# Performance work log

Hardware: AMD Instinct MI355X
Metric: run time of the kernel (lower is better)

Reference implementation:

```python
import jax, jax.numpy as jnp
import numpy as np

B, Q, K, H, D = 2, 2048, 2048, 16, 64


def setup_inputs() -> dict:
    key = jax.random.key(0)
    k1, k2, k3, k4 = jax.random.split(key, 4)
    qs = jax.random.normal(k1, (B, Q, H, D), dtype=jnp.float32)
    ks = jax.random.normal(k2, (B, K, H, D), dtype=jnp.float32)
    vs = jax.random.normal(k3, (B, K, H, D), dtype=jnp.float32)
    # valid lengths in [1, K] so no row is fully masked
    valid_lens = jax.random.randint(k4, (B,), 1, K + 1, dtype=jnp.int32)
    return {"qs": qs, "ks": ks, "vs": vs, "valid_lens": valid_lens}


def reference(qs, ks, vs, valid_lens):
    # Flash-attention-2 scan computes exact softmax attention with key masking;
    # the dense, numerically-stable equivalent:
    d = qs.shape[-1]
    scale = 1.0 / jnp.sqrt(jnp.asarray(d, dtype=qs.dtype))
    # scores: [B, H, Q, K]
    scores = jnp.einsum("bqhd,bkhd->bhqk", qs * scale, ks)
    kpos = jnp.arange(ks.shape[1])
    ks_mask = kpos[None, :] < valid_lens[:, None]            # [B, K]
    scores = jnp.where(ks_mask[:, None, None, :], scores, -jnp.inf)
    attn = jax.nn.softmax(scores, axis=-1)                   # stable online-softmax equivalent
    out = jnp.einsum("bhqk,bkhd->bqhd", attn, vs)            # [B, Q, H, D]
    return out
```

## Files before the change

### kernel.cpp

```cpp
#include <hip/hip_runtime.h>

#define B_ 2
#define Q_ 2048
#define K_ 2048
#define H_ 16
#define D_ 64
#define HD_ (H_ * D_)

#define QSCALE 0.18033688011112042f
#define DEFER_THR 10.0f

typedef __bf16 bf16_t;
typedef __attribute__((ext_vector_type(8))) __bf16 bf16x8;
typedef __attribute__((ext_vector_type(4))) __bf16 bf16x4;
typedef __attribute__((ext_vector_type(4))) float f32x4;

#define SBAR() do {                                         \
    __builtin_amdgcn_sched_barrier(0);                      \
    asm volatile("s_waitcnt lgkmcnt(0)" ::: "memory");      \
    __builtin_amdgcn_s_barrier();                           \
    __builtin_amdgcn_sched_barrier(0);                      \
} while (0)

__device__ __forceinline__ int swz(int row, int colByte) {
    return (row * 128 + colByte) ^ ((row & 7) << 4);
}

__global__ __launch_bounds__(512, 4) void attn_fwd_kernel(
    const float* __restrict__ qs, const float* __restrict__ ks,
    const float* __restrict__ vs, const int* __restrict__ valid_lens,
    float* __restrict__ out)
{
    const int qt   = blockIdx.x;
    const int h    = blockIdx.y;
    const int b    = blockIdx.z;
    const int tid  = threadIdx.x;
    const int wave = tid >> 6;
    const int lane = tid & 63;
    const int l16  = lane & 15;
    const int lhi  = lane >> 4;

    const int valid  = valid_lens[b];
    const int ntiles = (valid + 63) >> 6;

    __shared__ bf16_t k_lds[2][64 * 64];
    __shared__ bf16_t v_lds[2][64 * 64];
    __shared__ bf16_t p_buf[8][16 * 64];
    char* const pbase = (char*)&p_buf[wave][0];

    const int    qrow = qt * 128 + wave * 16 + l16;
    const float* qp   = qs + (((size_t)b * Q_ + qrow) * H_ + h) * D_;
    bf16x8 a_q[2];
    #pragma unroll
    for (int dh = 0; dh < 2; ++dh) {
        const f32x4* q4 = (const f32x4*)(qp + dh * 32 + lhi * 8);
        f32x4 lo = q4[0], hi = q4[1];
        #pragma unroll
        for (int j = 0; j < 4; ++j) {
            a_q[dh][j]     = (bf16_t)(lo[j] * QSCALE);
            a_q[dh][4 + j] = (bf16_t)(hi[j] * QSCALE);
        }
    }

    f32x4 o_acc[4];
    #pragma unroll
    for (int t = 0; t < 4; ++t) o_acc[t] = (f32x4){0.f, 0.f, 0.f, 0.f};
    float m_r = -1e30f, l_part = 0.f;

    const float* kb = ks + ((size_t)b * K_ * H_ + h) * D_;
    const float* vg = vs + ((size_t)b * K_ * H_ + h) * D_;

    const bool kRole = (tid < 256);
    const int  st    = kRole ? tid : (tid - 256);
    const int  krow  = st >> 2;
    const int  kcolf = (st & 3) * 16;
    const int  vr    = (st & 15) * 4;
    const int  vc    = (st >> 4) * 4;

    f32x4 reg[4];

    auto issue_loads = [&](int kt) {
        if (kRole) {
            const float* ksrc = kb + (size_t)(kt * 64 + krow) * HD_ + kcolf;
            #pragma unroll
            for (int i = 0; i < 4; ++i) reg[i] = ((const f32x4*)ksrc)[i];
        } else {
            #pragma unroll
            for (int i = 0; i < 4; ++i)
                reg[i] = *(const f32x4*)(vg + (size_t)(kt * 64 + vr + i) * HD_ + vc);
        }
    };

    auto write_tile = [&](int bi) {
        if (kRole) {
            char* kdst = (char*)&k_lds[bi][0];
            bf16x8 lo, hi;
            #pragma unroll
            for (int j = 0; j < 4; ++j) {
                lo[j] = (bf16_t)reg[0][j]; lo[4 + j] = (bf16_t)reg[1][j];
                hi[j] = (bf16_t)reg[2][j]; hi[4 + j] = (bf16_t)reg[3][j];
            }
            *(bf16x8*)(kdst + swz(krow, kcolf * 2))      = lo;
            *(bf16x8*)(kdst + swz(krow, kcolf * 2 + 16)) = hi;
        } else {
            char* vdst = (char*)&v_lds[bi][0];
            #pragma unroll
            for (int j = 0; j < 4; ++j) {
                bf16x4 w;
                w[0] = (bf16_t)reg[0][j]; w[1] = (bf16_t)reg[1][j];
                w[2] = (bf16_t)reg[2][j]; w[3] = (bf16_t)reg[3][j];
                *(bf16x4*)(vdst + swz(vc + j, vr * 2)) = w;
            }
        }
    };

    issue_loads(0);
    write_tile(0);
    int cur = 0;

    for (int kt = 0; kt < ntiles; ++kt) {
        const bool more = (kt + 1 < ntiles);
        if (more) issue_loads(kt + 1);
        SBAR();

        char* const kbase = (char*)&k_lds[cur][0];
        char* const vbase = (char*)&v_lds[cur][0];

        f32x4 s[4];
        #pragma unroll
        for (int n = 0; n < 4; ++n) s[n] = (f32x4){0.f, 0.f, 0.f, 0.f};
        __builtin_amdgcn_s_setprio(1);
        #pragma unroll
        for (int n = 0; n < 4; ++n) {
            #pragma unroll
            for (int dh = 0; dh < 2; ++dh) {
                bf16x8 ak = *(const bf16x8*)(kbase + swz(n * 16 + l16, dh * 64 + lhi * 16));
                s[n] = __builtin_amdgcn_mfma_f32_16x16x32_bf16(ak, a_q[dh], s[n], 0, 0, 0);
            }
        }
        __builtin_amdgcn_s_setprio(0);

        if (kt * 64 + 64 > valid) {
            #pragma unroll
            for (int n = 0; n < 4; ++n) {
                const int kbase_i = kt * 64 + n * 16 + lhi * 4;
                #pragma unroll
                for (int r = 0; r < 4; ++r)
                    if (kbase_i + r >= valid) s[n][r] = -1e30f;
            }
        }

        float lm = s[0][0];
        #pragma unroll
        for (int n = 0; n < 4; ++n)
            #pragma unroll
            for (int r = 0; r < 4; ++r) lm = fmaxf(lm, s[n][r]);
        if (__any(lm > m_r + DEFER_THR)) {
            float rm = fmaxf(lm, __shfl_xor(lm, 16, 64));
            rm = fmaxf(rm, __shfl_xor(rm, 32, 64));
            const float mnew  = fmaxf(m_r, rm);
            const float alpha = __builtin_amdgcn_exp2f(m_r - mnew);
            m_r = mnew;
            l_part *= alpha;
            #pragma unroll
            for (int t = 0; t < 4; ++t) o_acc[t] *= alpha;
        }
        float psum = 0.f;
        #pragma unroll
        for (int n = 0; n < 4; ++n) {
            bf16x4 w;
            #pragma unroll
            for (int r = 0; r < 4; ++r) {
                const float e = __builtin_amdgcn_exp2f(s[n][r] - m_r);
                psum += e;
                w[r] = (bf16_t)e;
            }
            *(bf16x4*)(pbase + swz(l16, n * 32 + lhi * 8)) = w;
        }
        l_part += psum;

        bf16x8 pb[2];
        #pragma unroll
        for (int kk = 0; kk < 2; ++kk)
            pb[kk] = *(const bf16x8*)(pbase + swz(l16, kk * 64 + lhi * 16));

        __builtin_amdgcn_s_setprio(1);
        #pragma unroll
        for (int t = 0; t < 4; ++t) {
            #pragma unroll
            for (int kk = 0; kk < 2; ++kk) {
                bf16x8 vb = *(const bf16x8*)(vbase + swz(t * 16 + l16, kk * 64 + lhi * 16));
                o_acc[t] = __builtin_amdgcn_mfma_f32_16x16x32_bf16(vb, pb[kk], o_acc[t], 0, 0, 0);
            }
        }
        __builtin_amdgcn_s_setprio(0);

        if (more) write_tile(cur ^ 1);
        cur ^= 1;
    }

    float l = l_part;
    l += __shfl_xor(l, 16, 64);
    l += __shfl_xor(l, 32, 64);
    const float inv = 1.f / l;
    float* op = out + (((size_t)b * Q_ + qrow) * H_ + h) * D_;
    #pragma unroll
    for (int t = 0; t < 4; ++t) {
        f32x4 res = o_acc[t];
        #pragma unroll
        for (int r = 0; r < 4; ++r) res[r] *= inv;
        *(f32x4*)(op + t * 16 + lhi * 4) = res;
    }
}

extern "C" void kernel_launch(void* const* d_in, const int* in_sizes, int n_in,
                              void* d_out, int out_size, void* d_ws, size_t ws_size,
                              hipStream_t stream) {
    const float* qs = (const float*)d_in[0];
    const float* ks = (const float*)d_in[1];
    const float* vs = (const float*)d_in[2];
    const int*   vl = (const int*)d_in[3];
    float*       out = (float*)d_out;
    dim3 grid(Q_ / 128, H_, B_);
    attn_fwd_kernel<<<grid, 512, 0, stream>>>(qs, ks, vs, vl, out);
}
```

Measured before the change: 39.11 us.

## Split the key range in two and merge partial results in a combine kernel

Adds a split-K variant of the attention kernel. Each query tile's key tiles are divided into two halves handled by separate blocks, which doubles the grid from 512 to 1024 blocks. Each block writes unnormalized bf16 partial outputs plus its running max and sum to workspace, and a second kernel rescales and merges the two halves. The aim is more parallelism and better CU occupancy. In exchange it adds a second launch, extra global traffic for the partials, and bf16 rounding of the partial outputs. The old single-pass path remains as a fallback when the workspace is too small.

```diff
diff --git a/kernel.cpp b/kernel.cpp
--- a/kernel.cpp
+++ b/kernel.cpp
@@ -6,6 +6,7 @@
 #define H_ 16
 #define D_ 64
 #define HD_ (H_ * D_)
+#define BQH (B_ * Q_ * H_)
 
 #define QSCALE 0.18033688011112042f
 #define DEFER_THR 10.0f
@@ -26,12 +27,15 @@
     return (row * 128 + colByte) ^ ((row & 7) << 4);
 }
 
-__global__ __launch_bounds__(512, 4) void attn_fwd_kernel(
+template<bool SPLITK>
+__global__ __launch_bounds__(512, SPLITK ? 6 : 4) void attn_fwd_kernel(
     const float* __restrict__ qs, const float* __restrict__ ks,
     const float* __restrict__ vs, const int* __restrict__ valid_lens,
-    float* __restrict__ out)
+    float* __restrict__ out, bf16_t* __restrict__ po, float* __restrict__ ml)
 {
-    const int qt   = blockIdx.x;
+    int qt, split;
+    if constexpr (SPLITK) { qt = blockIdx.x >> 1; split = blockIdx.x & 1; }
+    else                  { qt = blockIdx.x;      split = 0; }
     const int h    = blockIdx.y;
     const int b    = blockIdx.z;
     const int tid  = threadIdx.x;
@@ -42,14 +46,29 @@
 
     const int valid  = valid_lens[b];
     const int ntiles = (valid + 63) >> 6;
+    int tbeg = 0, tend = ntiles;
+    if constexpr (SPLITK) {
+        const int half = (ntiles + 1) >> 1;
+        tbeg = split ? half : 0;
+        tend = split ? ntiles : half;
+    }
+
+    const int qrow = qt * 128 + wave * 16 + l16;
+    size_t mlslot = 0;
+    if constexpr (SPLITK) {
+        mlslot = ((((size_t)split * B_ + b) * Q_ + qrow) * H_ + h) * 2;
+        if (tbeg >= tend) {
+            if (lhi == 0) { ml[mlslot] = -1e30f; ml[mlslot + 1] = 0.f; }
+            return;
+        }
+    }
 
     __shared__ bf16_t k_lds[2][64 * 64];
     __shared__ bf16_t v_lds[2][64 * 64];
     __shared__ bf16_t p_buf[8][16 * 64];
     char* const pbase = (char*)&p_buf[wave][0];
 
-    const int    qrow = qt * 128 + wave * 16 + l16;
-    const float* qp   = qs + (((size_t)b * Q_ + qrow) * H_ + h) * D_;
+    const float* qp = qs + (((size_t)b * Q_ + qrow) * H_ + h) * D_;
     bf16x8 a_q[2];
     #pragma unroll
     for (int dh = 0; dh < 2; ++dh) {
@@ -114,12 +133,12 @@
         }
     };
 
-    issue_loads(0);
+    issue_loads(tbeg);
     write_tile(0);
     int cur = 0;
 
-    for (int kt = 0; kt < ntiles; ++kt) {
-        const bool more = (kt + 1 < ntiles);
+    for (int kt = tbeg; kt < tend; ++kt) {
+        const bool more = (kt + 1 < tend);
         if (more) issue_loads(kt + 1);
         SBAR();
 
@@ -202,15 +221,49 @@
     float l = l_part;
     l += __shfl_xor(l, 16, 64);
     l += __shfl_xor(l, 32, 64);
-    const float inv = 1.f / l;
-    float* op = out + (((size_t)b * Q_ + qrow) * H_ + h) * D_;
+    if constexpr (SPLITK) {
+        if (lhi == 0) { ml[mlslot] = m_r; ml[mlslot + 1] = l; }
+        bf16_t* pop = po + ((((size_t)split * B_ + b) * Q_ + qrow) * H_ + h) * D_;
+        #pragma unroll
+        for (int t = 0; t < 4; ++t) {
+            bf16x4 w;
+            #pragma unroll
+            for (int r = 0; r < 4; ++r) w[r] = (bf16_t)o_acc[t][r];
+            *(bf16x4*)(pop + t * 16 + lhi * 4) = w;
+        }
+    } else {
+        const float inv = 1.f / l;
+        float* op = out + (((size_t)b * Q_ + qrow) * H_ + h) * D_;
+        #pragma unroll
+        for (int t = 0; t < 4; ++t) {
+            f32x4 res = o_acc[t];
+            #pragma unroll
+            for (int r = 0; r < 4; ++r) res[r] *= inv;
+            *(f32x4*)(op + t * 16 + lhi * 4) = res;
+        }
+    }
+}
+
+__global__ __launch_bounds__(256) void attn_combine(
+    const bf16_t* __restrict__ po, const float* __restrict__ ml,
+    float* __restrict__ out)
+{
+    const int idx  = blockIdx.x * 256 + threadIdx.x;
+    const int dv   = idx & 15;
+    const int slot = idx >> 4;
+    const float2 ml0 = ((const float2*)ml)[slot];
+    const float2 ml1 = ((const float2*)ml)[BQH + slot];
+    const float M   = fmaxf(ml0.x, ml1.x);
+    const float c0  = exp2f(ml0.x - M);
+    const float c1  = exp2f(ml1.x - M);
+    const float inv = 1.f / (c0 * ml0.y + c1 * ml1.y);
+    bf16x4 p0 = *(const bf16x4*)(po + (size_t)slot * D_ + dv * 4);
+    bf16x4 p1 = *(const bf16x4*)(po + (size_t)BQH * D_ + (size_t)slot * D_ + dv * 4);
+    f32x4 o;
     #pragma unroll
-    for (int t = 0; t < 4; ++t) {
-        f32x4 res = o_acc[t];
-        #pragma unroll
-        for (int r = 0; r < 4; ++r) res[r] *= inv;
-        *(f32x4*)(op + t * 16 + lhi * 4) = res;
-    }
+    for (int r = 0; r < 4; ++r)
+        o[r] = (c0 * (float)p0[r] + c1 * (float)p1[r]) * inv;
+    *(f32x4*)(out + (size_t)slot * D_ + dv * 4) = o;
 }
 
 extern "C" void kernel_launch(void* const* d_in, const int* in_sizes, int n_in,
@@ -221,6 +274,15 @@
     const float* vs = (const float*)d_in[2];
     const int*   vl = (const int*)d_in[3];
     float*       out = (float*)d_out;
-    dim3 grid(Q_ / 128, H_, B_);
-    attn_fwd_kernel<<<grid, 512, 0, stream>>>(qs, ks, vs, vl, out);
-}
+
+    const size_t po_bytes = (size_t)2 * BQH * D_ * sizeof(bf16_t);
+    const size_t ml_bytes = (size_t)2 * BQH * 2 * sizeof(float);
+    if (ws_size >= po_bytes + ml_bytes) {
+        bf16_t* po = (bf16_t*)d_ws;
+        float*  ml = (float*)((char*)d_ws + po_bytes);
+        attn_fwd_kernel<true><<<dim3(32, 16, 2), 512, 0, stream>>>(qs, ks, vs, vl, nullptr, po, ml);
+        attn_combine<<<dim3((BQH * 16) / 256), 256, 0, stream>>>(po, ml, out);
+    } else {
+        attn_fwd_kernel<false><<<dim3(16, 16, 2), 512, 0, stream>>>(qs, ks, vs, vl, out, nullptr, nullptr);
+    }
+}
```

New measurement: 74.88 us. 91.4% more time.
